# Kernel optimization log

Hardware: AMD Instinct MI355X
Metric: run time of the kernel (lower is better)

Reference implementation:

```python
import jax, jax.numpy as jnp
import numpy as np

N_GAUSS = 3200          # 20*20*8 voxel-center pseudo points
FEAT_DIM = 17
RENDER_H, RENDER_W = 48, 88
GT_H, GT_W = 192, 352
VOXEL_SIZE = 0.8
PC_MIN = np.array([-8.0, -8.0, -3.2], np.float32)
PC_MAX = np.array([8.0, 8.0, 3.2], np.float32)
NUSC_FREQ = np.array([1163161, 2309034, 188743, 2997643, 20317180, 852476, 243808,
                      2457947, 497017, 2731022, 7224789, 214411435, 5565043,
                      63191967, 76098082, 128860031, 141625221, 2307405309], np.float64)


def setup_inputs() -> dict:
    key = jax.random.key(0)
    k1, k2 = jax.random.split(key, 2)
    # pseudo voxel-center grid (get_presudo_xyz): cell centers on a 20x20x8 grid
    gx = (np.arange(20) + 0.5) * VOXEL_SIZE + PC_MIN[0]
    gy = (np.arange(20) + 0.5) * VOXEL_SIZE + PC_MIN[1]
    gz = (np.arange(8) + 0.5) * VOXEL_SIZE + PC_MIN[2]
    X, Y, Z = np.meshgrid(gx, gy, gz, indexing='ij')
    pc_xyz = np.stack([X, Y, Z], -1).reshape(-1, 3).astype(np.float32)
    # distCUDA2 on a regular grid: mean sq dist to 3 NNs == voxel_size^2
    scales = np.full((N_GAUSS, 3), np.log(VOXEL_SIZE), np.float32)  # log(sqrt(v^2))
    rots = np.zeros((N_GAUSS, 4), np.float32); rots[:, 0] = 1.0  # identity quats
    # two cameras looking at the grid (z_cam > 0 for all points)
    vm0 = np.array([[1, 0, 0, 0], [0, -1, 0, 0], [0, 0, -1, 20], [0, 0, 0, 1]], np.float32)
    vm1 = np.array([[0, 1, 0, 0], [0, 0, -1, 0], [-1, 0, 0, 20], [0, 0, 0, 1]], np.float32)
    viewmats = np.stack([vm0, vm1])
    intr = np.array([[100.0, 50.0, RENDER_W / 2.0, RENDER_H / 2.0]] * 2, np.float32)
    cw = (1.0 / np.log(NUSC_FREQ[:17] + 0.001)).astype(np.float32)
    return {
        'voxel_feats': jax.random.normal(k1, (1, N_GAUSS, FEAT_DIM), jnp.float32),
        'opacity': jax.random.uniform(k2, (1, N_GAUSS, 1), jnp.float32),
        'pc_xyz': jnp.asarray(pc_xyz),
        'scales': jnp.asarray(scales),
        'rots': jnp.asarray(rots),
        'viewmats': jnp.asarray(viewmats),
        'intrinsics': jnp.asarray(intr),
        'class_weights': jnp.asarray(cw),
        'gt_sem': jax.random.randint(jax.random.fold_in(key, 1), (2, GT_H, GT_W), 0, 17, jnp.int32),
        'sem_mask': jax.random.randint(jax.random.fold_in(key, 2), (2, GT_H, GT_W), 0, 2, jnp.int32),
    }


def quat_to_rot(q):
    q = q / jnp.linalg.norm(q, axis=-1, keepdims=True)
    w, x, y, z = q[:, 0], q[:, 1], q[:, 2], q[:, 3]
    return jnp.stack([
        jnp.stack([1 - 2 * (y * y + z * z), 2 * (x * y - w * z), 2 * (x * z + w * y)], -1),
        jnp.stack([2 * (x * y + w * z), 1 - 2 * (x * x + z * z), 2 * (y * z - w * x)], -1),
        jnp.stack([2 * (x * z - w * y), 2 * (y * z + w * x), 1 - 2 * (x * x + y * y)], -1),
    ], -2)  # [N,3,3]


def nearest_resize(img, H, W):
    hi, wi = img.shape
    ri = (jnp.arange(H) * hi) // H
    ci = (jnp.arange(W) * wi) // W
    return img[ri][:, ci]


def render_feature_map(feats, opac, xyz, scale, Rq, viewmat, intr):
    fx, fy, cx, cy = intr[0], intr[1], intr[2], intr[3]
    Rw, t = viewmat[:3, :3], viewmat[:3, 3]
    p = xyz @ Rw.T + t                      # [N,3] camera-frame
    z = p[:, 2]
    valid = z > 0.2
    zc = jnp.maximum(z, 0.2)
    u = fx * p[:, 0] / zc + cx
    v = fy * p[:, 1] / zc + cy
    # 3D covariance: Rq diag(s^2) Rq^T, then to camera frame
    cov3d = jnp.einsum('nij,nj,nkj->nik', Rq, scale * scale, Rq)
    cov_c = jnp.einsum('ij,njk,lk->nil', Rw, cov3d, Rw)
    # projection Jacobian (EWA splatting)
    zero = jnp.zeros_like(zc)
    J = jnp.stack([
        jnp.stack([fx / zc, zero, -fx * p[:, 0] / (zc * zc)], -1),
        jnp.stack([zero, fy / zc, -fy * p[:, 1] / (zc * zc)], -1),
    ], -2)                                  # [N,2,3]
    cov2 = jnp.einsum('nij,njk,nlk->nil', J, cov_c, J)
    a = cov2[:, 0, 0] + 0.3
    b = cov2[:, 0, 1]
    c = cov2[:, 1, 1] + 0.3
    det = jnp.maximum(a * c - b * b, 1e-8)
    A, B, C = c / det, -b / det, a / det    # conic
    px = jnp.arange(RENDER_W, dtype=jnp.float32)
    py = jnp.arange(RENDER_H, dtype=jnp.float32)
    dx = px[None, :] - u[:, None]           # [N,W]
    dy = py[None, :] - v[:, None]           # [N,H]
    power = (-0.5 * (A[:, None, None] * dx[:, None, :] ** 2
                     + C[:, None, None] * dy[:, :, None] ** 2)
             - B[:, None, None] * dx[:, None, :] * dy[:, :, None])  # [N,H,W]
    power = jnp.minimum(power, 0.0)
    alpha = jnp.clip(opac[:, None, None] * jnp.exp(power), 0.0, 0.99)
    alpha = alpha * valid[:, None, None].astype(alpha.dtype)
    order = jnp.argsort(z)                  # front-to-back depth sort
    alpha = alpha[order]
    feats_s = feats[order]
    T = jnp.cumprod(1.0 - alpha, axis=0)
    T_excl = jnp.concatenate([jnp.ones_like(T[:1]), T[:-1]], axis=0)
    w = alpha * T_excl                      # composite weights [N,H,W]
    return jnp.einsum('nhw,nc->hwc', w, feats_s)  # [H,W,17]


def masked_weighted_ce(logits, gt, mask, cw):
    logp = jax.nn.log_softmax(logits, -1)
    nll = -jnp.take_along_axis(logp, gt[:, None], axis=1)[:, 0]
    wi = cw[gt] * mask
    return jnp.sum(wi * nll) / jnp.maximum(jnp.sum(wi), 1e-8)


def reference(voxel_feats, opacity, pc_xyz, scales, rots, viewmats, intrinsics,
              class_weights, gt_sem, sem_mask):
    scale = jnp.exp(scales)
    Rq = quat_to_rot(rots)
    B = voxel_feats.shape[0]
    n_cam = viewmats.shape[0]
    loss_batch = 0.0
    for b in range(B):
        feats = voxel_feats[b].reshape(-1, FEAT_DIM)
        opac = opacity[b].reshape(-1)
        loss_cam = 0.0
        for c in range(n_cam):
            img = render_feature_map(feats, opac, pc_xyz, scale, Rq,
                                     viewmats[c], intrinsics[c])
            logits = img.reshape(-1, FEAT_DIM)
            gt = nearest_resize(gt_sem[c], RENDER_H, RENDER_W).reshape(-1)
            m = nearest_resize(sem_mask[c], RENDER_H, RENDER_W).reshape(-1).astype(jnp.float32)
            loss_cam = loss_cam + masked_weighted_ce(logits, gt, m, class_weights)
        loss_batch = loss_batch + loss_cam / n_cam
    return loss_batch / B  # gaussian_sem_weight = 1.0
```

## Files before the change

kernel.cpp:

```cpp
#include <hip/hip_runtime.h>

#define NG 3200
#define NF 17
#define NFP 18
#define RH 48
#define RW 88
#define NPIX (RH*RW)
#define GTH 192
#define GTW 352
#define NCAM 2
#define CHUNK 64
#define NCHUNK 50
#define GPC 5
#define NGROUP 10

typedef float v2f __attribute__((ext_vector_type(2)));

#define Z_OFF    0
#define PU_OFF   (Z_OFF + NCAM*NG)
#define PS_OFF   (PU_OFF + NCAM*NG*6)
#define FS_OFF   (PS_OFF + NCAM*NG*6)
#define PT_OFF   (FS_OFF + NCAM*NG*NFP)
#define GP_OFF   (PT_OFF + NCAM*NCHUNK*18*NPIX)
#define ACC_OFF  (GP_OFF + NCAM*NGROUP*18*NPIX)

__global__ __launch_bounds__(256) void k_preproc(
    const float* __restrict__ opac, const float* __restrict__ xyz,
    const float* __restrict__ scales, const float* __restrict__ rots,
    const float* __restrict__ vm, const float* __restrict__ intr,
    float* __restrict__ ws)
{
  int idx = blockIdx.x*blockDim.x + threadIdx.x;
  if (idx >= NCAM*NG) return;
  int cam = idx / NG, g = idx % NG;

  float qw=rots[g*4+0], qx=rots[g*4+1], qy=rots[g*4+2], qz=rots[g*4+3];
  float qn = rsqrtf(qw*qw+qx*qx+qy*qy+qz*qz);
  qw*=qn; qx*=qn; qy*=qn; qz*=qn;
  float R[3][3];
  R[0][0]=1.f-2.f*(qy*qy+qz*qz); R[0][1]=2.f*(qx*qy-qw*qz); R[0][2]=2.f*(qx*qz+qw*qy);
  R[1][0]=2.f*(qx*qy+qw*qz); R[1][1]=1.f-2.f*(qx*qx+qz*qz); R[1][2]=2.f*(qy*qz-qw*qx);
  R[2][0]=2.f*(qx*qz-qw*qy); R[2][1]=2.f*(qy*qz+qw*qx); R[2][2]=1.f-2.f*(qx*qx+qy*qy);

  float s2[3];
  #pragma unroll
  for (int k=0;k<3;k++){ float s=expf(scales[g*3+k]); s2[k]=s*s; }

  float M[3][3];
  #pragma unroll
  for(int i=0;i<3;i++)
    #pragma unroll
    for(int j=0;j<3;j++)
      M[i][j] = R[i][0]*s2[0]*R[j][0] + R[i][1]*s2[1]*R[j][1] + R[i][2]*s2[2]*R[j][2];

  const float* Vm = vm + cam*16;
  float Rw[3][3], t[3];
  #pragma unroll
  for(int i=0;i<3;i++){
    #pragma unroll
    for(int j=0;j<3;j++) Rw[i][j]=Vm[i*4+j];
    t[i]=Vm[i*4+3];
  }

  float T1[3][3];
  #pragma unroll
  for(int i=0;i<3;i++)
    #pragma unroll
    for(int j=0;j<3;j++)
      T1[i][j] = Rw[i][0]*M[0][j] + Rw[i][1]*M[1][j] + Rw[i][2]*M[2][j];
  float V[3][3];
  #pragma unroll
  for(int i=0;i<3;i++)
    #pragma unroll
    for(int j=0;j<3;j++)
      V[i][j] = T1[i][0]*Rw[j][0] + T1[i][1]*Rw[j][1] + T1[i][2]*Rw[j][2];

  float X=xyz[g*3+0], Y=xyz[g*3+1], Zp=xyz[g*3+2];
  float p0 = Rw[0][0]*X + Rw[0][1]*Y + Rw[0][2]*Zp + t[0];
  float p1 = Rw[1][0]*X + Rw[1][1]*Y + Rw[1][2]*Zp + t[1];
  float p2 = Rw[2][0]*X + Rw[2][1]*Y + Rw[2][2]*Zp + t[2];

  float z  = p2;
  float zc = fmaxf(z, 0.2f);
  float fx=intr[cam*4+0], fy=intr[cam*4+1], cx=intr[cam*4+2], cy=intr[cam*4+3];
  float u = fx*p0/zc + cx;
  float v = fy*p1/zc + cy;

  float j00 = fx/zc, j02 = -fx*p0/(zc*zc);
  float j11 = fy/zc, j12 = -fy*p1/(zc*zc);
  float c00 = j00*j00*V[0][0] + 2.f*j00*j02*V[0][2] + j02*j02*V[2][2];
  float c01 = j00*(V[0][1]*j11 + V[0][2]*j12) + j02*(V[2][1]*j11 + V[2][2]*j12);
  float c11 = j11*j11*V[1][1] + 2.f*j11*j12*V[1][2] + j12*j12*V[2][2];

  float a = c00 + 0.3f, b = c01, c = c11 + 0.3f;
  float det = fmaxf(a*c - b*b, 1e-8f);
  float A = c/det, Bc = -b/det, C = a/det;
  float opv = (z > 0.2f) ? opac[g] : 0.0f;

  ws[Z_OFF + idx] = z;
  float* P = ws + PU_OFF + (size_t)idx*6;
  P[0]=u; P[1]=v; P[2]=A; P[3]=Bc; P[4]=C; P[5]=opv;
}

__global__ __launch_bounds__(256) void k_sort(
    const float* __restrict__ feats, float* __restrict__ ws)
{
  __shared__ float zsh[NG];
  int cam = blockIdx.y;
  for (int i=threadIdx.x; i<NG; i+=256) zsh[i] = ws[Z_OFF + cam*NG + i];
  __syncthreads();

  int wave = threadIdx.x >> 6, lane = threadIdx.x & 63;
  int g = blockIdx.x*4 + wave;
  float zi = zsh[g];
  int rank = 0;
  #pragma unroll 5
  for (int k=0; k<NG/64; k++){
    int j = k*64 + lane;
    float zj = zsh[j];
    rank += ((zj < zi) || (zj == zi && j < g)) ? 1 : 0;
  }
  #pragma unroll
  for (int off=32; off>0; off>>=1) rank += __shfl_down(rank, off, 64);
  rank = __shfl(rank, 0, 64);

  const float* src = ws + PU_OFF + (size_t)(cam*NG+g)*6;
  if (lane < 6) (ws + PS_OFF + (size_t)(cam*NG+rank)*6)[lane] = src[lane];
  if (lane < NFP) (ws + FS_OFF + (size_t)(cam*NG+rank)*NFP)[lane] =
                     (lane < NF) ? feats[g*NF+lane] : 0.0f;
}

__global__ __launch_bounds__(256) void k_render(float* __restrict__ ws)
{
  __shared__ float sp[CHUNK*6];
  __shared__ v2f   sf2[CHUNK*(NFP/2)];
  int cam = blockIdx.z, chunk = blockIdx.y;
  int g0 = chunk*CHUNK;
  const float* psrc = ws + PS_OFF + (size_t)(cam*NG+g0)*6;
  for (int i=threadIdx.x; i<CHUNK*6; i+=256) sp[i]=psrc[i];
  const float* fsrc = ws + FS_OFF + (size_t)(cam*NG+g0)*NFP;
  float* sff = (float*)sf2;
  for (int i=threadIdx.x; i<CHUNK*NFP; i+=256) sff[i]=fsrc[i];
  __syncthreads();

  int pix = blockIdx.x*256 + threadIdx.x;
  if (pix >= NPIX) return;
  float px = (float)(pix % RW), py = (float)(pix / RW);

  float T = 1.0f;
  v2f F2[9];
  #pragma unroll
  for(int k=0;k<9;k++) F2[k]=(v2f)(0.f);

  #pragma unroll 4
  for (int g=0; g<CHUNK; g++){
    const float* P = sp + g*6;
    float dx = px - P[0], dy = py - P[1];
    float power = -0.5f*(P[2]*dx*dx + P[4]*dy*dy) - P[3]*dx*dy;
    power = fminf(power, 0.f);
    float alpha = fminf(P[5]*__expf(power), 0.99f);
    float w = alpha*T;
    T *= (1.f - alpha);
    v2f w2; w2.x = w; w2.y = w;
    const v2f* f2 = sf2 + g*(NFP/2);
    #pragma unroll
    for(int k=0;k<9;k++) F2[k] += w2*f2[k];
  }

  float* out = ws + PT_OFF + (size_t)((cam*NCHUNK+chunk)*18)*NPIX + pix;
  const float* Ff = (const float*)F2;
  #pragma unroll
  for(int k=0;k<NF;k++) out[k*NPIX]=Ff[k];
  out[17*NPIX]=T;
}

__global__ __launch_bounds__(256) void k_combine(float* __restrict__ ws)
{
  int cam = blockIdx.z, grp = blockIdx.y;
  int pix = blockIdx.x*256 + threadIdx.x;
  if (pix >= NPIX) return;
  float F[NF];
  #pragma unroll
  for(int k=0;k<NF;k++) F[k]=0.f;
  float T = 1.f;
  for (int c=grp*GPC; c<grp*GPC+GPC; c++){
    const float* base = ws + PT_OFF + (size_t)((cam*NCHUNK+c)*18)*NPIX + pix;
    #pragma unroll
    for(int k=0;k<NF;k++) F[k] += T*base[k*NPIX];
    T *= base[17*NPIX];
  }
  float* out = ws + GP_OFF + (size_t)((cam*NGROUP+grp)*18)*NPIX + pix;
  #pragma unroll
  for(int k=0;k<NF;k++) out[k*NPIX]=F[k];
  out[17*NPIX]=T;
}

__global__ __launch_bounds__(256) void k_loss(
    const int* __restrict__ gt, const int* __restrict__ mask,
    const float* __restrict__ cw, float* __restrict__ ws)
{
  int cam = blockIdx.y;
  int pix = blockIdx.x*256 + threadIdx.x;
  float num = 0.f, den = 0.f;
  if (pix < NPIX) {
    float img[NF];
    #pragma unroll
    for(int k=0;k<NF;k++) img[k]=0.f;
    float Trun = 1.f;
    for (int c=0; c<NGROUP; c++){
      const float* base = ws + GP_OFF + (size_t)((cam*NGROUP+c)*18)*NPIX + pix;
      #pragma unroll
      for(int k=0;k<NF;k++) img[k] += Trun*base[k*NPIX];
      Trun *= base[17*NPIX];
    }
    int row = pix / RW, col = pix % RW;
    int gofs = cam*GTH*GTW + (row*4)*GTW + col*4;
    int gi = gt[gofs];
    float mi = (float)mask[gofs];
    float mx = img[0];
    #pragma unroll
    for(int k=1;k<NF;k++) mx = fmaxf(mx, img[k]);
    float s = 0.f;
    #pragma unroll
    for(int k=0;k<NF;k++) s += expf(img[k]-mx);
    float lse = mx + logf(s);
    float nll = lse - img[gi];
    float wi  = cw[gi]*mi;
    num = wi*nll; den = wi;
  }
  #pragma unroll
  for (int off=32; off>0; off>>=1){
    num += __shfl_down(num, off, 64);
    den += __shfl_down(den, off, 64);
  }
  if ((threadIdx.x & 63) == 0){
    atomicAdd(ws + ACC_OFF + cam*2 + 0, num);
    atomicAdd(ws + ACC_OFF + cam*2 + 1, den);
  }
}

__global__ void k_final(const float* __restrict__ ws, float* __restrict__ out)
{
  float l0 = ws[ACC_OFF+0]/fmaxf(ws[ACC_OFF+1], 1e-8f);
  float l1 = ws[ACC_OFF+2]/fmaxf(ws[ACC_OFF+3], 1e-8f);
  out[0] = 0.5f*(l0 + l1);
}

extern "C" void kernel_launch(void* const* d_in, const int* in_sizes, int n_in,
                              void* d_out, int out_size, void* d_ws, size_t ws_size,
                              hipStream_t stream) {
  const float* vf   = (const float*)d_in[0];
  const float* op   = (const float*)d_in[1];
  const float* xyz  = (const float*)d_in[2];
  const float* sc   = (const float*)d_in[3];
  const float* rt   = (const float*)d_in[4];
  const float* vm   = (const float*)d_in[5];
  const float* intr = (const float*)d_in[6];
  const float* cw   = (const float*)d_in[7];
  const int*   gt   = (const int*)d_in[8];
  const int*   mask = (const int*)d_in[9];
  float* ws  = (float*)d_ws;
  float* out = (float*)d_out;

  hipMemsetAsync(ws + ACC_OFF, 0, 4*sizeof(float), stream);
  k_preproc<<<dim3((NCAM*NG+255)/256), 256, 0, stream>>>(op, xyz, sc, rt, vm, intr, ws);
  k_sort   <<<dim3(NG/4, NCAM), 256, 0, stream>>>(vf, ws);
  k_render <<<dim3((NPIX+255)/256, NCHUNK, NCAM), 256, 0, stream>>>(ws);
  k_combine<<<dim3((NPIX+255)/256, NGROUP, NCAM), 256, 0, stream>>>(ws);
  k_loss   <<<dim3((NPIX+255)/256, NCAM), 256, 0, stream>>>(gt, mask, cw, ws);
  k_final  <<<1,1,0,stream>>>(ws, out);
}
```

Measured before the change: 152.9 us.

## Store partial render planes in fp16, prefold exp2 constants, resize blocks to 192

Partial per-chunk and per-group feature and transmittance planes are now stored as packed half2 (9 planes instead of 18 floats), halving intermediate memory traffic between render, combine and loss. The conic coefficients are prescaled by -0.5*log2(e) so the inner loop uses FMAs and exp2f. Block size changes to 192 so NPIX divides evenly and bounds checks are dropped. The accumulator zeroing moves into k_preproc, removing the memset. fp16 storage of transmittance and features loses precision in the composited loss.

Result: faster. 130.5 us (-14.6%).

```diff
diff --git a/kernel.cpp b/kernel.cpp
--- a/kernel.cpp
+++ b/kernel.cpp
@@ -13,16 +13,18 @@
 #define NCHUNK 50
 #define GPC 5
 #define NGROUP 10
+#define NPL 9
 
 typedef float v2f __attribute__((ext_vector_type(2)));
+typedef _Float16 h2 __attribute__((ext_vector_type(2)));
 
 #define Z_OFF    0
 #define PU_OFF   (Z_OFF + NCAM*NG)
 #define PS_OFF   (PU_OFF + NCAM*NG*6)
 #define FS_OFF   (PS_OFF + NCAM*NG*6)
 #define PT_OFF   (FS_OFF + NCAM*NG*NFP)
-#define GP_OFF   (PT_OFF + NCAM*NCHUNK*18*NPIX)
-#define ACC_OFF  (GP_OFF + NCAM*NGROUP*18*NPIX)
+#define GP_OFF   (PT_OFF + NCAM*NCHUNK*NPL*NPIX)
+#define ACC_OFF  (GP_OFF + NCAM*NGROUP*NPL*NPIX)
 
 __global__ __launch_bounds__(256) void k_preproc(
     const float* __restrict__ opac, const float* __restrict__ xyz,
@@ -31,6 +33,7 @@
     float* __restrict__ ws)
 {
   int idx = blockIdx.x*blockDim.x + threadIdx.x;
+  if (idx < 4) ws[ACC_OFF + idx] = 0.0f;
   if (idx >= NCAM*NG) return;
   int cam = idx / NG, g = idx % NG;
 
@@ -94,12 +97,15 @@
 
   float a = c00 + 0.3f, b = c01, c = c11 + 0.3f;
   float det = fmaxf(a*c - b*b, 1e-8f);
-  float A = c/det, Bc = -b/det, C = a/det;
+  const float L2E = 1.4426950408889634f;
+  float A2 = -0.5f*L2E * (c/det);
+  float B2 = -L2E * (-b/det);
+  float C2 = -0.5f*L2E * (a/det);
   float opv = (z > 0.2f) ? opac[g] : 0.0f;
 
   ws[Z_OFF + idx] = z;
   float* P = ws + PU_OFF + (size_t)idx*6;
-  P[0]=u; P[1]=v; P[2]=A; P[3]=Bc; P[4]=C; P[5]=opv;
+  P[0]=u; P[1]=v; P[2]=A2; P[3]=B2; P[4]=C2; P[5]=opv;
 }
 
 __global__ __launch_bounds__(256) void k_sort(
@@ -130,21 +136,20 @@
                      (lane < NF) ? feats[g*NF+lane] : 0.0f;
 }
 
-__global__ __launch_bounds__(256) void k_render(float* __restrict__ ws)
+__global__ __launch_bounds__(192) void k_render(float* __restrict__ ws)
 {
   __shared__ float sp[CHUNK*6];
   __shared__ v2f   sf2[CHUNK*(NFP/2)];
   int cam = blockIdx.z, chunk = blockIdx.y;
   int g0 = chunk*CHUNK;
   const float* psrc = ws + PS_OFF + (size_t)(cam*NG+g0)*6;
-  for (int i=threadIdx.x; i<CHUNK*6; i+=256) sp[i]=psrc[i];
+  for (int i=threadIdx.x; i<CHUNK*6; i+=192) sp[i]=psrc[i];
   const float* fsrc = ws + FS_OFF + (size_t)(cam*NG+g0)*NFP;
   float* sff = (float*)sf2;
-  for (int i=threadIdx.x; i<CHUNK*NFP; i+=256) sff[i]=fsrc[i];
+  for (int i=threadIdx.x; i<CHUNK*NFP; i+=192) sff[i]=fsrc[i];
   __syncthreads();
 
-  int pix = blockIdx.x*256 + threadIdx.x;
-  if (pix >= NPIX) return;
+  int pix = blockIdx.x*192 + threadIdx.x;
   float px = (float)(pix % RW), py = (float)(pix / RW);
 
   float T = 1.0f;
@@ -156,78 +161,91 @@
   for (int g=0; g<CHUNK; g++){
     const float* P = sp + g*6;
     float dx = px - P[0], dy = py - P[1];
-    float power = -0.5f*(P[2]*dx*dx + P[4]*dy*dy) - P[3]*dx*dy;
-    power = fminf(power, 0.f);
-    float alpha = fminf(P[5]*__expf(power), 0.99f);
+    float m1 = P[2]*dx;
+    float m2 = fmaf(P[3], dy, m1);
+    float m3 = dx*m2;
+    float power2 = fmaf(P[4]*dy, dy, m3);
+    power2 = fminf(power2, 0.f);
+    float alpha = fminf(P[5]*exp2f(power2), 0.99f);
     float w = alpha*T;
-    T *= (1.f - alpha);
+    T = fmaf(-alpha, T, T);
     v2f w2; w2.x = w; w2.y = w;
     const v2f* f2 = sf2 + g*(NFP/2);
     #pragma unroll
     for(int k=0;k<9;k++) F2[k] += w2*f2[k];
   }
 
-  float* out = ws + PT_OFF + (size_t)((cam*NCHUNK+chunk)*18)*NPIX + pix;
   const float* Ff = (const float*)F2;
-  #pragma unroll
-  for(int k=0;k<NF;k++) out[k*NPIX]=Ff[k];
-  out[17*NPIX]=T;
-}
-
-__global__ __launch_bounds__(256) void k_combine(float* __restrict__ ws)
+  h2* out = (h2*)(ws + PT_OFF) + (size_t)((cam*NCHUNK+chunk)*NPL)*NPIX + pix;
+  #pragma unroll
+  for(int k=0;k<8;k++){
+    h2 v; v.x = (_Float16)Ff[2*k]; v.y = (_Float16)Ff[2*k+1];
+    out[k*NPIX] = v;
+  }
+  { h2 v; v.x = (_Float16)Ff[16]; v.y = (_Float16)T; out[8*NPIX] = v; }
+}
+
+__global__ __launch_bounds__(192) void k_combine(float* __restrict__ ws)
 {
   int cam = blockIdx.z, grp = blockIdx.y;
-  int pix = blockIdx.x*256 + threadIdx.x;
-  if (pix >= NPIX) return;
+  int pix = blockIdx.x*192 + threadIdx.x;
   float F[NF];
   #pragma unroll
   for(int k=0;k<NF;k++) F[k]=0.f;
   float T = 1.f;
   for (int c=grp*GPC; c<grp*GPC+GPC; c++){
-    const float* base = ws + PT_OFF + (size_t)((cam*NCHUNK+c)*18)*NPIX + pix;
-    #pragma unroll
-    for(int k=0;k<NF;k++) F[k] += T*base[k*NPIX];
-    T *= base[17*NPIX];
-  }
-  float* out = ws + GP_OFF + (size_t)((cam*NGROUP+grp)*18)*NPIX + pix;
-  #pragma unroll
-  for(int k=0;k<NF;k++) out[k*NPIX]=F[k];
-  out[17*NPIX]=T;
-}
-
-__global__ __launch_bounds__(256) void k_loss(
+    const h2* base = (const h2*)(ws + PT_OFF) + (size_t)((cam*NCHUNK+c)*NPL)*NPIX + pix;
+    h2 v[9];
+    #pragma unroll
+    for(int k=0;k<9;k++) v[k] = base[k*NPIX];
+    #pragma unroll
+    for(int k=0;k<8;k++){ F[2*k] += T*(float)v[k].x; F[2*k+1] += T*(float)v[k].y; }
+    F[16] += T*(float)v[8].x;
+    T *= (float)v[8].y;
+  }
+  h2* out = (h2*)(ws + GP_OFF) + (size_t)((cam*NGROUP+grp)*NPL)*NPIX + pix;
+  #pragma unroll
+  for(int k=0;k<8;k++){
+    h2 v; v.x = (_Float16)F[2*k]; v.y = (_Float16)F[2*k+1];
+    out[k*NPIX] = v;
+  }
+  { h2 v; v.x = (_Float16)F[16]; v.y = (_Float16)T; out[8*NPIX] = v; }
+}
+
+__global__ __launch_bounds__(192) void k_loss(
     const int* __restrict__ gt, const int* __restrict__ mask,
     const float* __restrict__ cw, float* __restrict__ ws)
 {
   int cam = blockIdx.y;
-  int pix = blockIdx.x*256 + threadIdx.x;
-  float num = 0.f, den = 0.f;
-  if (pix < NPIX) {
-    float img[NF];
-    #pragma unroll
-    for(int k=0;k<NF;k++) img[k]=0.f;
-    float Trun = 1.f;
-    for (int c=0; c<NGROUP; c++){
-      const float* base = ws + GP_OFF + (size_t)((cam*NGROUP+c)*18)*NPIX + pix;
-      #pragma unroll
-      for(int k=0;k<NF;k++) img[k] += Trun*base[k*NPIX];
-      Trun *= base[17*NPIX];
-    }
-    int row = pix / RW, col = pix % RW;
-    int gofs = cam*GTH*GTW + (row*4)*GTW + col*4;
-    int gi = gt[gofs];
-    float mi = (float)mask[gofs];
-    float mx = img[0];
-    #pragma unroll
-    for(int k=1;k<NF;k++) mx = fmaxf(mx, img[k]);
-    float s = 0.f;
-    #pragma unroll
-    for(int k=0;k<NF;k++) s += expf(img[k]-mx);
-    float lse = mx + logf(s);
-    float nll = lse - img[gi];
-    float wi  = cw[gi]*mi;
-    num = wi*nll; den = wi;
-  }
+  int pix = blockIdx.x*192 + threadIdx.x;
+  float img[NF];
+  #pragma unroll
+  for(int k=0;k<NF;k++) img[k]=0.f;
+  float Trun = 1.f;
+  for (int c=0; c<NGROUP; c++){
+    const h2* base = (const h2*)(ws + GP_OFF) + (size_t)((cam*NGROUP+c)*NPL)*NPIX + pix;
+    h2 v[9];
+    #pragma unroll
+    for(int k=0;k<9;k++) v[k] = base[k*NPIX];
+    #pragma unroll
+    for(int k=0;k<8;k++){ img[2*k] += Trun*(float)v[k].x; img[2*k+1] += Trun*(float)v[k].y; }
+    img[16] += Trun*(float)v[8].x;
+    Trun *= (float)v[8].y;
+  }
+  int row = pix / RW, col = pix % RW;
+  int gofs = cam*GTH*GTW + (row*4)*GTW + col*4;
+  int gi = gt[gofs];
+  float mi = (float)mask[gofs];
+  float mx = img[0];
+  #pragma unroll
+  for(int k=1;k<NF;k++) mx = fmaxf(mx, img[k]);
+  float s = 0.f;
+  #pragma unroll
+  for(int k=0;k<NF;k++) s += expf(img[k]-mx);
+  float lse = mx + logf(s);
+  float nll = lse - img[gi];
+  float wi  = cw[gi]*mi;
+  float num = wi*nll, den = wi;
   #pragma unroll
   for (int off=32; off>0; off>>=1){
     num += __shfl_down(num, off, 64);
@@ -262,11 +280,10 @@
   float* ws  = (float*)d_ws;
   float* out = (float*)d_out;
 
-  hipMemsetAsync(ws + ACC_OFF, 0, 4*sizeof(float), stream);
   k_preproc<<<dim3((NCAM*NG+255)/256), 256, 0, stream>>>(op, xyz, sc, rt, vm, intr, ws);
   k_sort   <<<dim3(NG/4, NCAM), 256, 0, stream>>>(vf, ws);
-  k_render <<<dim3((NPIX+255)/256, NCHUNK, NCAM), 256, 0, stream>>>(ws);
-  k_combine<<<dim3((NPIX+255)/256, NGROUP, NCAM), 256, 0, stream>>>(ws);
-  k_loss   <<<dim3((NPIX+255)/256, NCAM), 256, 0, stream>>>(gt, mask, cw, ws);
+  k_render <<<dim3(NPIX/192, NCHUNK, NCAM), 192, 0, stream>>>(ws);
+  k_combine<<<dim3(NPIX/192, NGROUP, NCAM), 192, 0, stream>>>(ws);
+  k_loss   <<<dim3(NPIX/192, NCAM), 192, 0, stream>>>(gt, mask, cw, ws);
   k_final  <<<1,1,0,stream>>>(ws, out);
 }
```
